# Kernel tuning notes

Hardware: AMD Instinct MI355X
Metric: run time of the kernel (lower is better)

Reference implementation:

```python
import jax, jax.numpy as jnp
import numpy as np

N_NODES = 100000
N_EDGES = 1600000
IN_CH = 128
OUT_CH = 128
EDGE_DIM = 6
STATE_DIM = 5


def setup_inputs() -> dict:
    key = jax.random.key(0)
    k = jax.random.split(key, 8)
    x = jax.random.normal(k[0], (N_NODES, IN_CH), dtype=jnp.float32)
    edge_index = jax.random.randint(k[1], (2, N_EDGES), 0, N_NODES, dtype=jnp.int64)
    edge_attr = jax.random.normal(k[2], (N_EDGES, EDGE_DIM), dtype=jnp.float32)
    global_state = jax.random.normal(k[3], (N_NODES, STATE_DIM), dtype=jnp.float32)
    # learned params (glorot init for weights, zero bias like torch default-ish)
    d_neg_in = IN_CH + EDGE_DIM + STATE_DIM
    d_root_in = IN_CH + STATE_DIM
    s_neg = jnp.sqrt(6.0 / (d_neg_in + OUT_CH))
    s_root = jnp.sqrt(6.0 / (d_root_in + OUT_CH))
    W_neg = jax.random.uniform(k[4], (d_neg_in, OUT_CH), jnp.float32, -s_neg, s_neg)
    b_neg = jax.random.uniform(k[5], (OUT_CH,), jnp.float32, -0.05, 0.05)
    W_root = jax.random.uniform(k[6], (d_root_in, OUT_CH), jnp.float32, -s_root, s_root)
    b_root = jax.random.uniform(k[7], (OUT_CH,), jnp.float32, -0.05, 0.05)
    return {"x": x, "edge_index": edge_index, "edge_attr": edge_attr,
            "global_state": global_state, "W_neg": W_neg, "b_neg": b_neg,
            "W_root": W_root, "b_root": b_root}


def reference(x, edge_index, edge_attr, global_state, W_neg, b_neg, W_root, b_root):
    # x: [N, C], global_state: [N, S]
    xs = jnp.concatenate([x, global_state], axis=1)            # [N, C+S]
    src = xs[edge_index[1]]                                    # gather: [E, C+S]
    x_adj = jnp.concatenate([src, edge_attr], axis=1)          # [E, C+S+Ed]
    x_adj = jax.nn.elu(x_adj @ W_neg + b_neg)                  # [E, O]
    neg_sum = jax.ops.segment_sum(x_adj, edge_index[0], num_segments=xs.shape[0])  # [N, O]
    x_out = jax.nn.elu(xs @ W_root + b_root) + neg_sum         # [N, O]
    return x_out
```

## Files before the change

kernel.cpp:

```cpp
#include <hip/hip_runtime.h>
#include <hip/hip_bf16.h>
#include <math.h>

#define N_NODES 100000
#define N_EDGES 1600000
#define IN_CH 128
#define OUT_CH 128
#define EDGE_DIM 6
#define STATE_DIM 5
#define XS_DIM 133
#define KPAD 160
#define NKSTEP 5
#define ASTRIDE 168
#define NBLK 391
#define N_CHUNKS 25000
#define NGB 1563
#define NHB 1601

typedef short s16x8 __attribute__((ext_vector_type(8)));
typedef float f32x4 __attribute__((ext_vector_type(4)));
typedef float f32x2 __attribute__((ext_vector_type(2)));
typedef unsigned u32x4 __attribute__((ext_vector_type(4)));

static __device__ __forceinline__ unsigned short f2bf(float f) {
    __hip_bfloat16 h = __float2bfloat16(f);
    return *reinterpret_cast<unsigned short*>(&h);
}
static __device__ __forceinline__ float bflo(unsigned u) {
    return __uint_as_float(u << 16);
}
static __device__ __forceinline__ float bfhi(unsigned u) {
    return __uint_as_float(u & 0xffff0000u);
}

__global__ __launch_bounds__(64) void repack_w(
    const float* __restrict__ Wneg, const float* __restrict__ Wroot,
    unsigned short* __restrict__ Pneg, unsigned short* __restrict__ Proot)
{
    int b = blockIdx.x;
    int mat = b / 40, r = b % 40;
    int kk = r / 8, nt = r % 8;
    int lane = threadIdx.x;
    const float* W = mat ? Wroot : Wneg;
    unsigned short* P = mat ? Proot : Pneg;
    int n = nt * 16 + (lane & 15);
    int kb = kk * 32 + (lane >> 4) * 8;
    unsigned short v[8];
#pragma unroll
    for (int j = 0; j < 8; ++j) {
        int k = kb + j;
        v[j] = (k < XS_DIM) ? f2bf(W[k * 128 + n]) : (unsigned short)0;
    }
    *(s16x8*)(P + ((size_t)(kk * 8 + nt) * 64 + lane) * 8) = *(s16x8*)v;
}

__global__ __launch_bounds__(256) void gemm_hist(
    const float* __restrict__ x, const float* __restrict__ gs,
    const unsigned short* __restrict__ Pneg, const unsigned short* __restrict__ Proot,
    const float* __restrict__ bneg, const float* __restrict__ broot,
    __hip_bfloat16* __restrict__ Yb, float* __restrict__ out,
    const int* __restrict__ idx, int* __restrict__ cnt)
{
    __shared__ unsigned short Alds[64 * ASTRIDE];
    const int bid = blockIdx.x;
    int role, rid;
    if (bid < 2 * NGB) { role = bid & 1; rid = bid >> 1; }
    else               { role = 1;       rid = NGB + (bid - 2 * NGB); }

    const int tid  = threadIdx.x;

    if (role == 1) {
        for (int e = rid * 256 + tid; e < N_EDGES; e += NHB * 256) {
            int d = __builtin_nontemporal_load(idx + e);
            atomicAdd(&cnt[d], 1);
        }
        return;
    }

    const int lane = tid & 63;
    const int wv   = tid >> 6;
    const int n0   = rid * 64;

#pragma unroll
    for (int i = 0; i < 16; ++i) {
        int row = i * 4 + wv;
        int nn  = min(n0 + row, N_NODES - 1);
        const f32x2 v = __builtin_nontemporal_load(
            (const f32x2*)(x + (size_t)nn * IN_CH) + lane);
        unsigned pk = (unsigned)f2bf(v.x) | ((unsigned)f2bf(v.y) << 16);
        *(unsigned*)(&Alds[row * ASTRIDE + lane * 2]) = pk;
    }
#pragma unroll
    for (int s2 = 0; s2 < 4; ++s2) {
        int slot = tid * 4 + s2;
        int row  = slot >> 4;
        int cp   = slot & 15;
        int nn   = min(n0 + row, N_NODES - 1);
        int c0   = IN_CH + cp * 2;
        unsigned lo = (c0     < XS_DIM) ? (unsigned)f2bf(gs[(size_t)nn * STATE_DIM + (c0 - IN_CH)])     : 0u;
        unsigned hi = (c0 + 1 < XS_DIM) ? (unsigned)f2bf(gs[(size_t)nn * STATE_DIM + (c0 + 1 - IN_CH)]) : 0u;
        *(unsigned*)(&Alds[row * ASTRIDE + c0]) = lo | (hi << 16);
    }
    __syncthreads();

    f32x4 accN[8], accR[8];
    const f32x4 zero = {0.f, 0.f, 0.f, 0.f};
#pragma unroll
    for (int nt = 0; nt < 8; ++nt) { accN[nt] = zero; accR[nt] = zero; }

    const int m = lane & 15, quad = lane >> 4;
    const unsigned short* arow = Alds + (wv * 16 + m) * ASTRIDE + quad * 8;

    for (int kk = 0; kk < NKSTEP; ++kk) {
        s16x8 a = *(const s16x8*)(arow + kk * 32);
        const unsigned short* bp = Pneg  + ((size_t)kk * 8 * 64 + lane) * 8;
        const unsigned short* rp = Proot + ((size_t)kk * 8 * 64 + lane) * 8;
#pragma unroll
        for (int nt = 0; nt < 8; ++nt) {
            s16x8 bn = *(const s16x8*)(bp + nt * 512);
            accN[nt] = __builtin_amdgcn_mfma_f32_16x16x32_bf16(a, bn, accN[nt], 0, 0, 0);
            s16x8 br = *(const s16x8*)(rp + nt * 512);
            accR[nt] = __builtin_amdgcn_mfma_f32_16x16x32_bf16(a, br, accR[nt], 0, 0, 0);
        }
    }

#pragma unroll
    for (int nt = 0; nt < 8; ++nt) {
        int col = nt * 16 + m;
        float bn = bneg[col], br = broot[col];
        int rbase = n0 + wv * 16 + quad * 4;
#pragma unroll
        for (int r = 0; r < 4; ++r) {
            int node = rbase + r;
            if (node < N_NODES) {
                Yb[(size_t)node * 128 + col] = __float2bfloat16(accN[nt][r] + bn);
                float v = accR[nt][r] + br;
                out[(size_t)node * 128 + col] = (v > 0.f) ? v : (__expf(v) - 1.f);
            }
        }
    }
}

__global__ __launch_bounds__(256) void scan_block_sums(const int* __restrict__ cnt,
                                                       int* __restrict__ bsum) {
    __shared__ int ws[4];
    int tid = threadIdx.x, lane = tid & 63, wid = tid >> 6;
    int i = blockIdx.x * 256 + tid;
    int v = (i < N_NODES) ? cnt[i] : 0;
#pragma unroll
    for (int d = 32; d > 0; d >>= 1) v += __shfl_down(v, d);
    if (lane == 0) ws[wid] = v;
    __syncthreads();
    if (tid == 0) bsum[blockIdx.x] = ws[0] + ws[1] + ws[2] + ws[3];
}

__global__ __launch_bounds__(512) void scan_bsums(int* __restrict__ bsum) {
    __shared__ int s[512];
    int tid = threadIdx.x;
    int v = (tid < NBLK) ? bsum[tid] : 0;
    s[tid] = v;
    __syncthreads();
    for (int d = 1; d < 512; d <<= 1) {
        int t = (tid >= d) ? s[tid - d] : 0;
        __syncthreads();
        s[tid] += t;
        __syncthreads();
    }
    if (tid < NBLK) bsum[tid] = s[tid] - v;
}

__global__ __launch_bounds__(256) void scan_final(const int* __restrict__ cnt,
                                                  const int* __restrict__ bsum,
                                                  int* __restrict__ off,
                                                  int* __restrict__ cursor,
                                                  int* __restrict__ chunk_node) {
    __shared__ int wsum[4];
    int tid = threadIdx.x, lane = tid & 63, wid = tid >> 6;
    int i = blockIdx.x * 256 + tid;
    int v = (i < N_NODES) ? cnt[i] : 0;
    int x = v;
#pragma unroll
    for (int d = 1; d < 64; d <<= 1) {
        int t = __shfl_up(x, d);
        if (lane >= d) x += t;
    }
    if (lane == 63) wsum[wid] = x;
    __syncthreads();
    int wpre = 0;
#pragma unroll
    for (int j = 0; j < 4; ++j) wpre += (j < wid) ? wsum[j] : 0;
    int excl = bsum[blockIdx.x] + wpre + x - v;
    if (i < N_NODES) {
        off[i] = excl; cursor[i] = excl;
        if (v > 0) {
            int end = excl + v;
            for (int c = (excl + 63) >> 6; (c << 6) < end; ++c)
                chunk_node[c] = i;
        }
    }
}

__global__ __launch_bounds__(256) void scatter_edges(const int* __restrict__ idx,
                                                     const float* __restrict__ ea,
                                                     int* __restrict__ cursor,
                                                     uint4* __restrict__ pay) {
    int e = blockIdx.x * 256 + threadIdx.x;
    if (e < N_EDGES) {
        int dst = __builtin_nontemporal_load(idx + e);
        int src = __builtin_nontemporal_load(idx + N_EDGES + e);
        const f32x2* er = (const f32x2*)(ea + (size_t)e * EDGE_DIM);
        f32x2 e01 = __builtin_nontemporal_load(er);
        f32x2 e23 = __builtin_nontemporal_load(er + 1);
        f32x2 e45 = __builtin_nontemporal_load(er + 2);
        unsigned p0 = (unsigned)f2bf(e01.x) | ((unsigned)f2bf(e01.y) << 16);
        unsigned p1 = (unsigned)f2bf(e23.x) | ((unsigned)f2bf(e23.y) << 16);
        unsigned p2 = (unsigned)f2bf(e45.x) | ((unsigned)f2bf(e45.y) << 16);
        int pos = atomicAdd(&cursor[dst], 1);
        u32x4 pl = { (unsigned)src, p0, p1, p2 };
        __builtin_nontemporal_store(pl, (u32x4*)pay + pos);
    }
}

__global__ __launch_bounds__(256) void aggregate(
    const uint4* __restrict__ pay,
    const float* __restrict__ Wneg,
    const __hip_bfloat16* __restrict__ Yb,
    const int* __restrict__ off,
    const int* __restrict__ chunk_node,
    float* __restrict__ out)
{
    const int lane = threadIdx.x & 63;
    const int wid  = __builtin_amdgcn_readfirstlane(blockIdx.x * 4 + (threadIdx.x >> 6));
    const int e0   = wid * 64;

    const float2* wb2 = (const float2*)(Wneg + 133 * 128);
    float2 wb[EDGE_DIM];
#pragma unroll
    for (int j = 0; j < EDGE_DIM; ++j) wb[j] = wb2[j * 64 + lane];

    const unsigned* Yu = (const unsigned*)Yb;

    u32x4 pl = __builtin_nontemporal_load((const u32x4*)pay + e0 + lane);
    int src_l = (int)pl.x;
    int ea0 = (int)pl.y, ea1 = (int)pl.z, ea2 = (int)pl.w;

    int n   = __builtin_amdgcn_readfirstlane(chunk_node[wid]);
    int nxt = __builtin_amdgcn_readfirstlane((n + 1 < N_NODES) ? off[n + 1] : N_EDGES);

    float accx = 0.f, accy = 0.f;

    unsigned yA[8], yB[8];
#pragma unroll
    for (int j = 0; j < 8; ++j) {
        int s = __builtin_amdgcn_readlane(src_l, j);
        yA[j] = Yu[(size_t)s * 64 + lane];
    }
#pragma unroll
    for (int j = 0; j < 8; ++j) {
        int s = __builtin_amdgcn_readlane(src_l, 8 + j);
        yB[j] = Yu[(size_t)s * 64 + lane];
    }

    auto edge_op = [&](unsigned yv, int c, bool last) {
        unsigned a0 = (unsigned)__builtin_amdgcn_readlane(ea0, c);
        unsigned a1 = (unsigned)__builtin_amdgcn_readlane(ea1, c);
        unsigned a2 = (unsigned)__builtin_amdgcn_readlane(ea2, c);
        float f0 = bflo(a0), f1 = bfhi(a0);
        float f2 = bflo(a1), f3 = bfhi(a1);
        float f4 = bflo(a2), f5 = bfhi(a2);
        float tx = bflo(yv), ty = bfhi(yv);
        tx = fmaf(f0, wb[0].x, tx); ty = fmaf(f0, wb[0].y, ty);
        tx = fmaf(f1, wb[1].x, tx); ty = fmaf(f1, wb[1].y, ty);
        tx = fmaf(f2, wb[2].x, tx); ty = fmaf(f2, wb[2].y, ty);
        tx = fmaf(f3, wb[3].x, tx); ty = fmaf(f3, wb[3].y, ty);
        tx = fmaf(f4, wb[4].x, tx); ty = fmaf(f4, wb[4].y, ty);
        tx = fmaf(f5, wb[5].x, tx); ty = fmaf(f5, wb[5].y, ty);
        tx = (tx > 0.f) ? tx : (__expf(tx) - 1.f);
        ty = (ty > 0.f) ? ty : (__expf(ty) - 1.f);
        accx += tx; accy += ty;
        int e = e0 + c;
        bool bend = (e + 1 == nxt);
        if (last || bend) {
            float* orow = out + ((size_t)n << 7) + (lane << 1);
            atomicAdd(orow,     accx);
            atomicAdd(orow + 1, accy);
            accx = 0.f; accy = 0.f;
            if (!last) {
                n++;
                nxt = __builtin_amdgcn_readfirstlane(
                    (n + 1 < N_NODES) ? off[n + 1] : N_EDGES);
                while (nxt <= e + 1) {
                    n++;
                    nxt = __builtin_amdgcn_readfirstlane(
                        (n + 1 < N_NODES) ? off[n + 1] : N_EDGES);
                }
            }
        }
    };

#pragma unroll 1
    for (int q = 0; q < 3; ++q) {
        const int base = q * 16;
        const int pb   = base + 16;
#pragma unroll
        for (int j = 0; j < 8; ++j) {
            edge_op(yA[j], base + j, false);
            int s = __builtin_amdgcn_readlane(src_l, pb + j);
            yA[j] = Yu[(size_t)s * 64 + lane];
        }
#pragma unroll
        for (int j = 0; j < 8; ++j) {
            edge_op(yB[j], base + 8 + j, false);
            int s = __builtin_amdgcn_readlane(src_l, pb + 8 + j);
            yB[j] = Yu[(size_t)s * 64 + lane];
        }
    }
#pragma unroll
    for (int j = 0; j < 8; ++j) edge_op(yA[j], 48 + j, false);
#pragma unroll
    for (int j = 0; j < 8; ++j) edge_op(yB[j], 56 + j, j == 7);
}

extern "C" void kernel_launch(void* const* d_in, const int* in_sizes, int n_in,
                              void* d_out, int out_size, void* d_ws, size_t ws_size,
                              hipStream_t stream) {
    const float* x     = (const float*)d_in[0];
    const int*   idx   = (const int*)  d_in[1];
    const float* ea    = (const float*)d_in[2];
    const float* gs    = (const float*)d_in[3];
    const float* Wneg  = (const float*)d_in[4];
    const float* bneg  = (const float*)d_in[5];
    const float* Wroot = (const float*)d_in[6];
    const float* broot = (const float*)d_in[7];
    float* out = (float*)d_out;

    char* w = (char*)d_ws;
    __hip_bfloat16* Yb = (__hip_bfloat16*)w;      w += (size_t)N_NODES * 128 * 2;
    int* cnt  = (int*)w;                          w += (size_t)N_NODES * 4;
    int* off  = (int*)w;                          w += (size_t)N_NODES * 4;
    int* cur  = (int*)w;                          w += (size_t)N_NODES * 4;
    int* bsum = (int*)w;                          w += 2048;
    uint4* pay = (uint4*)w;                       w += (size_t)N_EDGES * 16;
    unsigned short* Pneg  = (unsigned short*)w;   w += (size_t)NKSTEP * 8 * 64 * 8 * 2;
    unsigned short* Proot = (unsigned short*)w;   w += (size_t)NKSTEP * 8 * 64 * 8 * 2;
    int* chunk_node = (int*)w;

    const int nb_edges = (N_EDGES + 255) / 256;

    hipMemsetAsync(cnt, 0, (size_t)N_NODES * 4, stream);
    repack_w<<<80, 64, 0, stream>>>(Wneg, Wroot, Pneg, Proot);
    gemm_hist<<<2 * NGB + (NHB - NGB), 256, 0, stream>>>(
        x, gs, Pneg, Proot, bneg, broot, Yb, out, idx, cnt);
    scan_block_sums<<<NBLK, 256, 0, stream>>>(cnt, bsum);
    scan_bsums<<<1, 512, 0, stream>>>(bsum);
    scan_final<<<NBLK, 256, 0, stream>>>(cnt, bsum, off, cur, chunk_node);
    scatter_edges<<<nb_edges, 256, 0, stream>>>(idx, ea, cur, pay);
    aggregate<<<N_CHUNKS / 4, 256, 0, stream>>>(pay, Wneg, Yb, off, chunk_node, out);
}
```

Before: 433.7 us.

## Overlap edge scatter with node GEMM and fold memset and bsum scan away

Reorders the pipeline: histogram and scan now run first, and the edge scatter into CSR payload is co-scheduled with the node GEMM in one kernel via interleaved block roles. The histogram is no longer overlapped with the GEMM. The memset is folded into the weight-repack kernel, and the single-block bsum scan is replaced by having each scan_final block sum its predecessors directly. This cuts the launch count by two. The intent is to hide the heavier scatter traffic behind GEMM work. The cost is that the histogram now runs standalone and each scan block does redundant prefix summation.

```diff
diff --git a/kernel.cpp b/kernel.cpp
--- a/kernel.cpp
+++ b/kernel.cpp
@@ -15,7 +15,6 @@
 #define NBLK 391
 #define N_CHUNKS 25000
 #define NGB 1563
-#define NHB 1601
 
 typedef short s16x8 __attribute__((ext_vector_type(8)));
 typedef float f32x4 __attribute__((ext_vector_type(4)));
@@ -33,14 +32,18 @@
     return __uint_as_float(u & 0xffff0000u);
 }
 
-__global__ __launch_bounds__(64) void repack_w(
+__global__ __launch_bounds__(64) void repack_zero(
     const float* __restrict__ Wneg, const float* __restrict__ Wroot,
-    unsigned short* __restrict__ Pneg, unsigned short* __restrict__ Proot)
+    unsigned short* __restrict__ Pneg, unsigned short* __restrict__ Proot,
+    int* __restrict__ cnt)
 {
     int b = blockIdx.x;
+    int lane = threadIdx.x;
+
+    for (int i = b * 64 + lane; i < N_NODES; i += 80 * 64) cnt[i] = 0;
+
     int mat = b / 40, r = b % 40;
     int kk = r / 8, nt = r % 8;
-    int lane = threadIdx.x;
     const float* W = mat ? Wroot : Wneg;
     unsigned short* P = mat ? Proot : Pneg;
     int n = nt * 16 + (lane & 15);
@@ -54,25 +57,100 @@
     *(s16x8*)(P + ((size_t)(kk * 8 + nt) * 64 + lane) * 8) = *(s16x8*)v;
 }
 
-__global__ __launch_bounds__(256) void gemm_hist(
+__global__ __launch_bounds__(256) void histogram(const int* __restrict__ idx,
+                                                 int* __restrict__ cnt) {
+    int e = blockIdx.x * 256 + threadIdx.x;
+    if (e < N_EDGES) {
+        int d = __builtin_nontemporal_load(idx + e);
+        atomicAdd(&cnt[d], 1);
+    }
+}
+
+__global__ __launch_bounds__(256) void scan_block_sums(const int* __restrict__ cnt,
+                                                       int* __restrict__ bsum) {
+    __shared__ int ws[4];
+    int tid = threadIdx.x, lane = tid & 63, wid = tid >> 6;
+    int i = blockIdx.x * 256 + tid;
+    int v = (i < N_NODES) ? cnt[i] : 0;
+#pragma unroll
+    for (int d = 32; d > 0; d >>= 1) v += __shfl_down(v, d);
+    if (lane == 0) ws[wid] = v;
+    __syncthreads();
+    if (tid == 0) bsum[blockIdx.x] = ws[0] + ws[1] + ws[2] + ws[3];
+}
+
+__global__ __launch_bounds__(256) void scan_final2(const int* __restrict__ cnt,
+                                                   const int* __restrict__ bsum,
+                                                   int* __restrict__ off,
+                                                   int* __restrict__ cursor,
+                                                   int* __restrict__ chunk_node) {
+    __shared__ int wsum[4];
+    __shared__ int bpre_s;
+    int tid = threadIdx.x, lane = tid & 63, wid = tid >> 6;
+    int bid = blockIdx.x;
+
+    int pre = 0;
+    for (int j = tid; j < bid; j += 256) pre += bsum[j];
+#pragma unroll
+    for (int d = 32; d > 0; d >>= 1) pre += __shfl_down(pre, d);
+    if (lane == 0) wsum[wid] = pre;
+    __syncthreads();
+    if (tid == 0) bpre_s = wsum[0] + wsum[1] + wsum[2] + wsum[3];
+    __syncthreads();
+    int bpre = bpre_s;
+
+    int i = bid * 256 + tid;
+    int v = (i < N_NODES) ? cnt[i] : 0;
+    int x = v;
+#pragma unroll
+    for (int d = 1; d < 64; d <<= 1) {
+        int t = __shfl_up(x, d);
+        if (lane >= d) x += t;
+    }
+    if (lane == 63) wsum[wid] = x;
+    __syncthreads();
+    int wpre = 0;
+#pragma unroll
+    for (int j = 0; j < 4; ++j) wpre += (j < wid) ? wsum[j] : 0;
+    int excl = bpre + wpre + x - v;
+    if (i < N_NODES) {
+        off[i] = excl; cursor[i] = excl;
+        if (v > 0) {
+            int end = excl + v;
+            for (int c = (excl + 63) >> 6; (c << 6) < end; ++c)
+                chunk_node[c] = i;
+        }
+    }
+}
+
+__global__ __launch_bounds__(256) void gemm_scatter(
     const float* __restrict__ x, const float* __restrict__ gs,
     const unsigned short* __restrict__ Pneg, const unsigned short* __restrict__ Proot,
     const float* __restrict__ bneg, const float* __restrict__ broot,
     __hip_bfloat16* __restrict__ Yb, float* __restrict__ out,
-    const int* __restrict__ idx, int* __restrict__ cnt)
+    const int* __restrict__ idx, const float* __restrict__ ea,
+    int* __restrict__ cursor, uint4* __restrict__ pay)
 {
     __shared__ unsigned short Alds[64 * ASTRIDE];
     const int bid = blockIdx.x;
-    int role, rid;
-    if (bid < 2 * NGB) { role = bid & 1; rid = bid >> 1; }
-    else               { role = 1;       rid = NGB + (bid - 2 * NGB); }
-
+    const int role = bid & 1;
+    const int rid  = bid >> 1;
     const int tid  = threadIdx.x;
 
     if (role == 1) {
-        for (int e = rid * 256 + tid; e < N_EDGES; e += NHB * 256) {
-            int d = __builtin_nontemporal_load(idx + e);
-            atomicAdd(&cnt[d], 1);
+        for (int e = rid * 256 + tid; e < N_EDGES; e += NGB * 256) {
+            int dst = __builtin_nontemporal_load(idx + e);
+            int src = __builtin_nontemporal_load(idx + N_EDGES + e);
+            const f32x2* er = (const f32x2*)(ea + (size_t)e * EDGE_DIM);
+            f32x2 e01 = __builtin_nontemporal_load(er);
+            f32x2 e23 = __builtin_nontemporal_load(er + 1);
+            f32x2 e45 = __builtin_nontemporal_load(er + 2);
+            unsigned p0 = (unsigned)f2bf(e01.x) | ((unsigned)f2bf(e01.y) << 16);
+            unsigned p1 = (unsigned)f2bf(e23.x) | ((unsigned)f2bf(e23.y) << 16);
+            unsigned p2 = (unsigned)f2bf(e45.x) | ((unsigned)f2bf(e45.y) << 16);
+            int pos = atomicAdd(&cursor[dst], 1);
+            u32x4 pl = { (unsigned)src, p0, p1, p2 };
+            __builtin_nontemporal_store(pl, (u32x4*)pay + pos);
         }
         return;
     }
@@ -138,86 +216,6 @@
                 out[(size_t)node * 128 + col] = (v > 0.f) ? v : (__expf(v) - 1.f);
             }
         }
-    }
-}
-
-__global__ __launch_bounds__(256) void scan_block_sums(const int* __restrict__ cnt,
-                                                       int* __restrict__ bsum) {
-    __shared__ int ws[4];
-    int tid = threadIdx.x, lane = tid & 63, wid = tid >> 6;
-    int i = blockIdx.x * 256 + tid;
-    int v = (i < N_NODES) ? cnt[i] : 0;
-#pragma unroll
-    for (int d = 32; d > 0; d >>= 1) v += __shfl_down(v, d);
-    if (lane == 0) ws[wid] = v;
-    __syncthreads();
-    if (tid == 0) bsum[blockIdx.x] = ws[0] + ws[1] + ws[2] + ws[3];
-}
-
-__global__ __launch_bounds__(512) void scan_bsums(int* __restrict__ bsum) {
-    __shared__ int s[512];
-    int tid = threadIdx.x;
-    int v = (tid < NBLK) ? bsum[tid] : 0;
-    s[tid] = v;
-    __syncthreads();
-    for (int d = 1; d < 512; d <<= 1) {
-        int t = (tid >= d) ? s[tid - d] : 0;
-        __syncthreads();
-        s[tid] += t;
-        __syncthreads();
-    }
-    if (tid < NBLK) bsum[tid] = s[tid] - v;
-}
-
-__global__ __launch_bounds__(256) void scan_final(const int* __restrict__ cnt,
-                                                  const int* __restrict__ bsum,
-                                                  int* __restrict__ off,
-                                                  int* __restrict__ cursor,
-                                                  int* __restrict__ chunk_node) {
-    __shared__ int wsum[4];
-    int tid = threadIdx.x, lane = tid & 63, wid = tid >> 6;
-    int i = blockIdx.x * 256 + tid;
-    int v = (i < N_NODES) ? cnt[i] : 0;
-    int x = v;
-#pragma unroll
-    for (int d = 1; d < 64; d <<= 1) {
-        int t = __shfl_up(x, d);
-        if (lane >= d) x += t;
-    }
-    if (lane == 63) wsum[wid] = x;
-    __syncthreads();
-    int wpre = 0;
-#pragma unroll
-    for (int j = 0; j < 4; ++j) wpre += (j < wid) ? wsum[j] : 0;
-    int excl = bsum[blockIdx.x] + wpre + x - v;
-    if (i < N_NODES) {
-        off[i] = excl; cursor[i] = excl;
-        if (v > 0) {
-            int end = excl + v;
-            for (int c = (excl + 63) >> 6; (c << 6) < end; ++c)
-                chunk_node[c] = i;
-        }
-    }
-}
-
-__global__ __launch_bounds__(256) void scatter_edges(const int* __restrict__ idx,
-                                                     const float* __restrict__ ea,
-                                                     int* __restrict__ cursor,
-                                                     uint4* __restrict__ pay) {
-    int e = blockIdx.x * 256 + threadIdx.x;
-    if (e < N_EDGES) {
-        int dst = __builtin_nontemporal_load(idx + e);
-        int src = __builtin_nontemporal_load(idx + N_EDGES + e);
-        const f32x2* er = (const f32x2*)(ea + (size_t)e * EDGE_DIM);
-        f32x2 e01 = __builtin_nontemporal_load(er);
-        f32x2 e23 = __builtin_nontemporal_load(er + 1);
-        f32x2 e45 = __builtin_nontemporal_load(er + 2);
-        unsigned p0 = (unsigned)f2bf(e01.x) | ((unsigned)f2bf(e01.y) << 16);
-        unsigned p1 = (unsigned)f2bf(e23.x) | ((unsigned)f2bf(e23.y) << 16);
-        unsigned p2 = (unsigned)f2bf(e45.x) | ((unsigned)f2bf(e45.y) << 16);
-        int pos = atomicAdd(&cursor[dst], 1);
-        u32x4 pl = { (unsigned)src, p0, p1, p2 };
-        __builtin_nontemporal_store(pl, (u32x4*)pay + pos);
     }
 }
 
@@ -347,13 +345,11 @@
 
     const int nb_edges = (N_EDGES + 255) / 256;
 
-    hipMemsetAsync(cnt, 0, (size_t)N_NODES * 4, stream);
-    repack_w<<<80, 64, 0, stream>>>(Wneg, Wroot, Pneg, Proot);
-    gemm_hist<<<2 * NGB + (NHB - NGB), 256, 0, stream>>>(
-        x, gs, Pneg, Proot, bneg, broot, Yb, out, idx, cnt);
+    repack_zero<<<80, 64, 0, stream>>>(Wneg, Wroot, Pneg, Proot, cnt);
+    histogram<<<nb_edges, 256, 0, stream>>>(idx, cnt);
     scan_block_sums<<<NBLK, 256, 0, stream>>>(cnt, bsum);
-    scan_bsums<<<1, 512, 0, stream>>>(bsum);
-    scan_final<<<NBLK, 256, 0, stream>>>(cnt, bsum, off, cur, chunk_node);
-    scatter_edges<<<nb_edges, 256, 0, stream>>>(idx, ea, cur, pay);
+    scan_final2<<<NBLK, 256, 0, stream>>>(cnt, bsum, off, cur, chunk_node);
+    gemm_scatter<<<2 * NGB, 256, 0, stream>>>(
+        x, gs, Pneg, Proot, bneg, broot, Yb, out, idx, ea, cur, pay);
     aggregate<<<N_CHUNKS / 4, 256, 0, stream>>>(pay, Wneg, Yb, off, chunk_node, out);
 }
```

After: 415.9 us. -4.1%, faster.
